# Kernel tuning notes

Hardware: AMD Instinct MI355X
Metric: run time of the kernel (lower is better)

## Reference

```python
import jax, jax.numpy as jnp
import numpy as np

D_MODEL = 1024
N_EXPERTS = 4
TOP_K = 32


def setup_inputs() -> dict:
    key = jax.random.key(0)
    k1, k2, k3, k4 = jax.random.split(key, 4)
    b, t, d = 2, 2048, D_MODEL
    n_lts = 8192
    h = jax.random.normal(k1, (b, t, d), dtype=jnp.float32)
    lts = jax.random.normal(k2, (1, n_lts, d), dtype=jnp.float32)
    # router: nn.Linear(d_model, n_experts)
    lim = 1.0 / np.sqrt(d)
    W_router = jax.random.uniform(k3, (N_EXPERTS, d), minval=-lim, maxval=lim, dtype=jnp.float32)
    b_router = jax.random.uniform(k4, (N_EXPERTS,), minval=-lim, maxval=lim, dtype=jnp.float32)
    return {"h": h, "lts": lts, "W_router": W_router, "b_router": b_router}


def reference(h, lts, W_router, b_router):
    b, t, d = h.shape
    n_lts = lts.shape[1]
    top_k = TOP_K
    n_experts = N_EXPERTS

    # router (eval mode: no noise)
    logits = jnp.einsum('btd,ed->bte', h, W_router) + b_router  # (b,t,E)
    expert_weights = jax.nn.softmax(logits, axis=-1)
    expert_idx = jnp.argmax(expert_weights, axis=-1)            # (b,t) int

    entries_per_expert = n_lts // n_experts
    offsets = jnp.minimum(expert_idx * entries_per_expert, n_lts - top_k)  # (b,t)
    indices = offsets[..., None] + jnp.arange(top_k)            # (b,t,k)
    indices = jnp.minimum(indices, n_lts - 1)

    # gather memory slices: lts broadcast over batch -> (b,t,k,d)
    selected = jnp.take(lts[0], indices, axis=0)

    # small attention of each token over its top_k memory entries
    scores = jnp.einsum('btd,btkd->btk', h, selected) / jnp.sqrt(jnp.asarray(d, h.dtype))
    attn = jax.nn.softmax(scores, axis=-1)
    result = jnp.einsum('btk,btkd->btd', attn, selected)
    return result, expert_weights
```

## Files before the change

### kernel.cpp

```cpp
#include <hip/hip_runtime.h>
#include <hip/hip_fp16.h>
#include <math.h>

constexpr int D    = 1024;
constexpr int NEXP = 4;
constexpr int EPP  = 2048;

typedef _Float16 f16x8 __attribute__((ext_vector_type(8)));
typedef float    f32x4 __attribute__((ext_vector_type(4)));

__device__ __forceinline__ unsigned pk2(float a, float b) {
    return __builtin_bit_cast(unsigned, __builtin_amdgcn_cvt_pkrtz(a, b));
}
__device__ __forceinline__ f16x8 cvt8(const float* p) {
    const float4 u = *reinterpret_cast<const float4*>(p);
    const float4 v = *reinterpret_cast<const float4*>(p + 4);
    const uint4 w = make_uint4(pk2(u.x, u.y), pk2(u.z, u.w), pk2(v.x, v.y), pk2(v.z, v.w));
    return __builtin_bit_cast(f16x8, w);
}

__global__ __launch_bounds__(256) void prep_router_kernel(
    const float* __restrict__ h, const float* __restrict__ lts,
    const float* __restrict__ Wr, const float* __restrict__ br,
    float* __restrict__ out_ew, int* __restrict__ eidx,
    _Float16* __restrict__ lts16, _Float16* __restrict__ ltsT, int ntok)
{
    const int tid = threadIdx.x;

    if (blockIdx.x < 64) {
        const int e = blockIdx.x >> 4, part = (blockIdx.x >> 2) & 3, dc = blockIdx.x & 3;
        __shared__ __align__(16) _Float16 s[8][256];

        const float4* src = reinterpret_cast<const float4*>(lts);
        #pragma unroll
        for (int i = 0; i < 2; ++i) {
            const int f = tid + 256 * i;
            const int r = f >> 6, c4 = f & 63;
            const float4 v = src[(size_t)(e * EPP + part * 8 + r) * 256 + dc * 64 + c4];
            *reinterpret_cast<uint2*>(&s[r][c4 * 4]) = make_uint2(pk2(v.x, v.y), pk2(v.z, v.w));
        }
        __syncthreads();

        {
            const int r = tid >> 5, c = tid & 31;
            *reinterpret_cast<uint4*>(lts16 + (size_t)(e * 32 + part * 8 + r) * D + dc * 256 + c * 8) =
                *reinterpret_cast<const uint4*>(&s[r][c * 8]);
        }
        {
            _Float16 tmp[8];
            #pragma unroll
            for (int k = 0; k < 8; ++k) tmp[k] = s[k][tid];
            *reinterpret_cast<uint4*>(ltsT + ((size_t)e << 15) + (size_t)(dc * 256 + tid) * 32 + part * 8) =
                *reinterpret_cast<const uint4*>(tmp);
        }
        return;
    }

    const int wid = tid >> 6, lane = tid & 63;
    const int tok = (blockIdx.x - 64) * 4 + wid;
    if (tok >= ntok) return;

    const float4* h4 = reinterpret_cast<const float4*>(h);
    const float4* w4 = reinterpret_cast<const float4*>(Wr);

    float acc[NEXP] = {0.f, 0.f, 0.f, 0.f};
    #pragma unroll
    for (int i = 0; i < 4; ++i) {
        const float4 a = h4[(size_t)tok * 256 + lane + 64 * i];
        #pragma unroll
        for (int e = 0; e < NEXP; ++e) {
            const float4 w = w4[e * 256 + lane + 64 * i];
            acc[e] += a.x * w.x + a.y * w.y + a.z * w.z + a.w * w.w;
        }
    }
    #pragma unroll
    for (int m = 1; m < 64; m <<= 1)
        #pragma unroll
        for (int e = 0; e < NEXP; ++e) acc[e] += __shfl_xor(acc[e], m);

    const float l0 = acc[0] + br[0], l1 = acc[1] + br[1],
                l2 = acc[2] + br[2], l3 = acc[3] + br[3];
    const float lm = fmaxf(fmaxf(l0, l1), fmaxf(l2, l3));
    const float e0 = __expf(l0 - lm), e1 = __expf(l1 - lm),
                e2 = __expf(l2 - lm), e3 = __expf(l3 - lm);
    const float einv = 1.f / (e0 + e1 + e2 + e3);
    if (lane < NEXP) {
        const float ev = (lane == 0) ? e0 : (lane == 1) ? e1 : (lane == 2) ? e2 : e3;
        out_ew[(size_t)tok * NEXP + lane] = ev * einv;
    }
    int bi = 0; float bv = l0;
    if (l1 > bv) { bv = l1; bi = 1; }
    if (l2 > bv) { bv = l2; bi = 2; }
    if (l3 > bv) { bv = l3; bi = 3; }
    if (lane == 0) eidx[tok] = bi;
}

__global__ __launch_bounds__(256) void qkpv_kernel(
    const float* __restrict__ h, const _Float16* __restrict__ lts16,
    const _Float16* __restrict__ ltsT, const int* __restrict__ eidx,
    float* __restrict__ out_res, int ntok, int chunks)
{
    const int e = blockIdx.x / chunks;
    const int chunk = blockIdx.x - e * chunks;
    const int base = chunk * 16;

    const int tid = threadIdx.x, wid = tid >> 6, lane = tid & 63;
    __shared__ int eix[16];
    __shared__ float S_part[4][16][33];
    __shared__ __align__(16) _Float16 P[16][32];

    if (tid < 16) {
        const int tk = base + tid;
        eix[tid] = (tk < ntok) ? eidx[tk] : -1;
    }

    const int rA = lane & 15, g4 = lane >> 4;
    int hr = base + rA; if (hr > ntok - 1) hr = ntok - 1;
    const float*     ap  = h     + (size_t)hr * D + g4 * 8;
    const _Float16* b0p = lts16 + (size_t)(e * 32 + rA) * D + g4 * 8;
    const _Float16* b1p = b0p + 16 * D;

    f32x4 s0 = {0.f, 0.f, 0.f, 0.f}, s1 = {0.f, 0.f, 0.f, 0.f};
    #pragma unroll
    for (int k = 0; k < 8; ++k) {
        const int kc = wid * 8 + k;
        const f16x8 a  = cvt8(ap + kc * 32);
        const f16x8 b0 = *reinterpret_cast<const f16x8*>(b0p + kc * 32);
        const f16x8 b1 = *reinterpret_cast<const f16x8*>(b1p + kc * 32);
        s0 = __builtin_amdgcn_mfma_f32_16x16x32_f16(a, b0, s0, 0, 0, 0);
        s1 = __builtin_amdgcn_mfma_f32_16x16x32_f16(a, b1, s1, 0, 0, 0);
    }
    #pragma unroll
    for (int r = 0; r < 4; ++r) {
        S_part[wid][g4 * 4 + r][rA]      = s0[r];
        S_part[wid][g4 * 4 + r][rA + 16] = s1[r];
    }
    __syncthreads();

    {
        const int tr = tid >> 4, sl = tid & 15;
        const float v0 = S_part[0][tr][sl] + S_part[1][tr][sl]
                       + S_part[2][tr][sl] + S_part[3][tr][sl];
        const float v1 = S_part[0][tr][sl + 16] + S_part[1][tr][sl + 16]
                       + S_part[2][tr][sl + 16] + S_part[3][tr][sl + 16];
        constexpr float inv32 = 1.f / 32.f;
        float mx = fmaxf(v0, v1);
        #pragma unroll
        for (int m = 1; m < 16; m <<= 1) mx = fmaxf(mx, __shfl_xor(mx, m));
        const float p0 = __expf((v0 - mx) * inv32);
        const float p1 = __expf((v1 - mx) * inv32);
        float sm = p0 + p1;
        #pragma unroll
        for (int m = 1; m < 16; m <<= 1) sm += __shfl_xor(sm, m);
        const float is = 1.f / sm;
        P[tr][sl]      = (_Float16)(p0 * is);
        P[tr][sl + 16] = (_Float16)(p1 * is);
    }
    __syncthreads();

    const f16x8 pa = *reinterpret_cast<const f16x8*>(&P[rA][g4 * 8]);
    const _Float16* vtE = ltsT + ((size_t)e << 15);

    #pragma unroll
    for (int i = 0; i < 16; ++i) {
        const int dimc = wid * 256 + i * 16 + rA;
        const f16x8 bk = *reinterpret_cast<const f16x8*>(vtE + (size_t)dimc * 32 + g4 * 8);
        f32x4 o = {0.f, 0.f, 0.f, 0.f};
        o = __builtin_amdgcn_mfma_f32_16x16x32_f16(pa, bk, o, 0, 0, 0);
        #pragma unroll
        for (int r = 0; r < 4; ++r) {
            const int tr2 = g4 * 4 + r;
            if (base + tr2 < ntok && eix[tr2] == e)
                out_res[(size_t)(base + tr2) * D + dimc] = o[r];
        }
    }
}

extern "C" void kernel_launch(void* const* d_in, const int* in_sizes, int n_in,
                              void* d_out, int out_size, void* d_ws, size_t ws_size,
                              hipStream_t stream) {
    const float* h   = (const float*)d_in[0];
    const float* lts = (const float*)d_in[1];
    const float* Wr  = (const float*)d_in[2];
    const float* br  = (const float*)d_in[3];

    const int ntok = in_sizes[0] / D;
    float* out_res = (float*)d_out;
    float* out_ew  = out_res + (size_t)ntok * D;

    _Float16* lts16 = (_Float16*)d_ws;
    _Float16* ltsT  = lts16 + (size_t)128 * D;
    int*      eidx  = (int*)(ltsT + (size_t)NEXP * D * 32);

    const int chunks = (ntok + 15) / 16;

    const int rblocks = 64 + (ntok + 3) / 4;
    prep_router_kernel<<<rblocks, 256, 0, stream>>>(h, lts, Wr, br, out_ew, eidx,
                                                    lts16, ltsT, ntok);
    qkpv_kernel<<<NEXP * chunks, 256, 0, stream>>>(h, lts16, ltsT, eidx,
                                                   out_res, ntok, chunks);
}
```

Measured before the change: 36.20 us.

## Fuse router computation into attention kernel, recomputing per expert block

Moves the router logits, softmax and argmax out of the prep kernel and into each qkpv block, which computes them for its own 16 tokens and writes expert weights only from the block whose expert matches. This removes the eidx global round trip and makes the prep kernel much smaller. The cost is that the router is recomputed four times, once per expert block, which adds extra reads of h and extra FLOPs plus a block-level sync before the MFMA phase.

```diff
diff --git a/kernel.cpp b/kernel.cpp
--- a/kernel.cpp
+++ b/kernel.cpp
@@ -19,86 +19,43 @@
     return __builtin_bit_cast(f16x8, w);
 }
 
-__global__ __launch_bounds__(256) void prep_router_kernel(
-    const float* __restrict__ h, const float* __restrict__ lts,
-    const float* __restrict__ Wr, const float* __restrict__ br,
-    float* __restrict__ out_ew, int* __restrict__ eidx,
-    _Float16* __restrict__ lts16, _Float16* __restrict__ ltsT, int ntok)
+__global__ __launch_bounds__(256) void prep_kernel(
+    const float* __restrict__ lts, _Float16* __restrict__ lts16,
+    _Float16* __restrict__ ltsT)
 {
+    const int e = blockIdx.x >> 4, part = (blockIdx.x >> 2) & 3, dc = blockIdx.x & 3;
     const int tid = threadIdx.x;
-
-    if (blockIdx.x < 64) {
-        const int e = blockIdx.x >> 4, part = (blockIdx.x >> 2) & 3, dc = blockIdx.x & 3;
-        __shared__ __align__(16) _Float16 s[8][256];
-
-        const float4* src = reinterpret_cast<const float4*>(lts);
-        #pragma unroll
-        for (int i = 0; i < 2; ++i) {
-            const int f = tid + 256 * i;
-            const int r = f >> 6, c4 = f & 63;
-            const float4 v = src[(size_t)(e * EPP + part * 8 + r) * 256 + dc * 64 + c4];
-            *reinterpret_cast<uint2*>(&s[r][c4 * 4]) = make_uint2(pk2(v.x, v.y), pk2(v.z, v.w));
-        }
-        __syncthreads();
-
-        {
-            const int r = tid >> 5, c = tid & 31;
-            *reinterpret_cast<uint4*>(lts16 + (size_t)(e * 32 + part * 8 + r) * D + dc * 256 + c * 8) =
-                *reinterpret_cast<const uint4*>(&s[r][c * 8]);
-        }
-        {
-            _Float16 tmp[8];
-            #pragma unroll
-            for (int k = 0; k < 8; ++k) tmp[k] = s[k][tid];
-            *reinterpret_cast<uint4*>(ltsT + ((size_t)e << 15) + (size_t)(dc * 256 + tid) * 32 + part * 8) =
-                *reinterpret_cast<const uint4*>(tmp);
-        }
-        return;
-    }
-
-    const int wid = tid >> 6, lane = tid & 63;
-    const int tok = (blockIdx.x - 64) * 4 + wid;
-    if (tok >= ntok) return;
-
-    const float4* h4 = reinterpret_cast<const float4*>(h);
-    const float4* w4 = reinterpret_cast<const float4*>(Wr);
-
-    float acc[NEXP] = {0.f, 0.f, 0.f, 0.f};
-    #pragma unroll
-    for (int i = 0; i < 4; ++i) {
-        const float4 a = h4[(size_t)tok * 256 + lane + 64 * i];
-        #pragma unroll
-        for (int e = 0; e < NEXP; ++e) {
-            const float4 w = w4[e * 256 + lane + 64 * i];
-            acc[e] += a.x * w.x + a.y * w.y + a.z * w.z + a.w * w.w;
-        }
-    }
-    #pragma unroll
-    for (int m = 1; m < 64; m <<= 1)
-        #pragma unroll
-        for (int e = 0; e < NEXP; ++e) acc[e] += __shfl_xor(acc[e], m);
-
-    const float l0 = acc[0] + br[0], l1 = acc[1] + br[1],
-                l2 = acc[2] + br[2], l3 = acc[3] + br[3];
-    const float lm = fmaxf(fmaxf(l0, l1), fmaxf(l2, l3));
-    const float e0 = __expf(l0 - lm), e1 = __expf(l1 - lm),
-                e2 = __expf(l2 - lm), e3 = __expf(l3 - lm);
-    const float einv = 1.f / (e0 + e1 + e2 + e3);
-    if (lane < NEXP) {
-        const float ev = (lane == 0) ? e0 : (lane == 1) ? e1 : (lane == 2) ? e2 : e3;
-        out_ew[(size_t)tok * NEXP + lane] = ev * einv;
-    }
-    int bi = 0; float bv = l0;
-    if (l1 > bv) { bv = l1; bi = 1; }
-    if (l2 > bv) { bv = l2; bi = 2; }
-    if (l3 > bv) { bv = l3; bi = 3; }
-    if (lane == 0) eidx[tok] = bi;
+    __shared__ __align__(16) _Float16 s[8][256];
+
+    const float4* src = reinterpret_cast<const float4*>(lts);
+    #pragma unroll
+    for (int i = 0; i < 2; ++i) {
+        const int f = tid + 256 * i;
+        const int r = f >> 6, c4 = f & 63;
+        const float4 v = src[(size_t)(e * EPP + part * 8 + r) * 256 + dc * 64 + c4];
+        *reinterpret_cast<uint2*>(&s[r][c4 * 4]) = make_uint2(pk2(v.x, v.y), pk2(v.z, v.w));
+    }
+    __syncthreads();
+
+    {
+        const int r = tid >> 5, c = tid & 31;
+        *reinterpret_cast<uint4*>(lts16 + (size_t)(e * 32 + part * 8 + r) * D + dc * 256 + c * 8) =
+            *reinterpret_cast<const uint4*>(&s[r][c * 8]);
+    }
+    {
+        _Float16 tmp[8];
+        #pragma unroll
+        for (int k = 0; k < 8; ++k) tmp[k] = s[k][tid];
+        *reinterpret_cast<uint4*>(ltsT + ((size_t)e << 15) + (size_t)(dc * 256 + tid) * 32 + part * 8) =
+            *reinterpret_cast<const uint4*>(tmp);
+    }
 }
 
 __global__ __launch_bounds__(256) void qkpv_kernel(
     const float* __restrict__ h, const _Float16* __restrict__ lts16,
-    const _Float16* __restrict__ ltsT, const int* __restrict__ eidx,
-    float* __restrict__ out_res, int ntok, int chunks)
+    const _Float16* __restrict__ ltsT, const float* __restrict__ Wr,
+    const float* __restrict__ br, float* __restrict__ out_res,
+    float* __restrict__ out_ew, int ntok, int chunks)
 {
     const int e = blockIdx.x / chunks;
     const int chunk = blockIdx.x - e * chunks;
@@ -109,14 +66,58 @@
     __shared__ float S_part[4][16][33];
     __shared__ __align__(16) _Float16 P[16][32];
 
-    if (tid < 16) {
-        const int tk = base + tid;
-        eix[tid] = (tk < ntok) ? eidx[tk] : -1;
-    }
+    {
+        const float4* h4 = reinterpret_cast<const float4*>(h);
+        const float4* w4 = reinterpret_cast<const float4*>(Wr);
+        float4 wf[NEXP][4];
+        #pragma unroll
+        for (int e2 = 0; e2 < NEXP; ++e2)
+            #pragma unroll
+            for (int i = 0; i < 4; ++i)
+                wf[e2][i] = w4[e2 * 256 + lane + 64 * i];
+        const float bb0 = br[0], bb1 = br[1], bb2 = br[2], bb3 = br[3];
+
+        #pragma unroll
+        for (int t = 0; t < 4; ++t) {
+            const int tok = base + wid * 4 + t;
+            if (tok < ntok) {
+                float acc[NEXP] = {0.f, 0.f, 0.f, 0.f};
+                #pragma unroll
+                for (int i = 0; i < 4; ++i) {
+                    const float4 a = h4[(size_t)tok * 256 + lane + 64 * i];
+                    #pragma unroll
+                    for (int e2 = 0; e2 < NEXP; ++e2)
+                        acc[e2] += a.x * wf[e2][i].x + a.y * wf[e2][i].y
+                                 + a.z * wf[e2][i].z + a.w * wf[e2][i].w;
+                }
+                #pragma unroll
+                for (int m = 1; m < 64; m <<= 1)
+                    #pragma unroll
+                    for (int e2 = 0; e2 < NEXP; ++e2) acc[e2] += __shfl_xor(acc[e2], m);
+
+                const float l0 = acc[0] + bb0, l1 = acc[1] + bb1,
+                            l2 = acc[2] + bb2, l3 = acc[3] + bb3;
+                const float lm = fmaxf(fmaxf(l0, l1), fmaxf(l2, l3));
+                const float e0 = __expf(l0 - lm), e1 = __expf(l1 - lm),
+                            e2v = __expf(l2 - lm), e3 = __expf(l3 - lm);
+                const float einv = 1.f / (e0 + e1 + e2v + e3);
+                int bi = 0; float bv = l0;
+                if (l1 > bv) { bv = l1; bi = 1; }
+                if (l2 > bv) { bv = l2; bi = 2; }
+                if (l3 > bv) { bv = l3; bi = 3; }
+                if (bi == e && lane < NEXP) {
+                    const float ev = (lane == 0) ? e0 : (lane == 1) ? e1 : (lane == 2) ? e2v : e3;
+                    out_ew[(size_t)tok * NEXP + lane] = ev * einv;
+                }
+                if (lane == 0) eix[wid * 4 + t] = bi;
+            } else if (lane == 0) eix[wid * 4 + t] = -1;
+        }
+    }
+    __syncthreads();
 
     const int rA = lane & 15, g4 = lane >> 4;
     int hr = base + rA; if (hr > ntok - 1) hr = ntok - 1;
-    const float*     ap  = h     + (size_t)hr * D + g4 * 8;
+    const float*    ap  = h     + (size_t)hr * D + g4 * 8;
     const _Float16* b0p = lts16 + (size_t)(e * 32 + rA) * D + g4 * 8;
     const _Float16* b1p = b0p + 16 * D;
 
@@ -190,13 +191,10 @@
 
     _Float16* lts16 = (_Float16*)d_ws;
     _Float16* ltsT  = lts16 + (size_t)128 * D;
-    int*      eidx  = (int*)(ltsT + (size_t)NEXP * D * 32);
 
     const int chunks = (ntok + 15) / 16;
 
-    const int rblocks = 64 + (ntok + 3) / 4;
-    prep_router_kernel<<<rblocks, 256, 0, stream>>>(h, lts, Wr, br, out_ew, eidx,
-                                                    lts16, ltsT, ntok);
-    qkpv_kernel<<<NEXP * chunks, 256, 0, stream>>>(h, lts16, ltsT, eidx,
-                                                   out_res, ntok, chunks);
-}
+    prep_kernel<<<64, 256, 0, stream>>>(lts, lts16, ltsT);
+    qkpv_kernel<<<NEXP * chunks, 256, 0, stream>>>(h, lts16, ltsT, Wr, br,
+                                                   out_res, out_ew, ntok, chunks);
+}
```

New measurement: 40.84 us. 12.8% more time.
